# Kernel optimization log

Hardware: AMD Instinct MI355X
Metric: run time of the kernel (lower is better)

## Reference

```python
import jax, jax.numpy as jnp
import numpy as np

EPS = 1e-5
K = 5  # sklearn NearestNeighbors(n_neighbors=5); includes the query point itself


def setup_inputs() -> dict:
    key = jax.random.key(0)
    points = jax.random.uniform(key, (16384, 3), dtype=jnp.float32)
    return {"points": points}


def _compute_lrfs(points):
    # Brute-force KNN (indices only; sklearn returns the self-point as nearest).
    sq = jnp.sum(points * points, axis=1)                      # [N]
    d2 = sq[:, None] + sq[None, :] - 2.0 * points @ points.T   # [N,N]
    _, nbh_idx = jax.lax.top_k(-jax.lax.stop_gradient(d2), K)  # [N,K] (indices only -> no grad path)

    diffs = points[nbh_idx] - points[:, None, :]               # [N,K,3]  (nbh = points[idx] - point)
    centered = diffs - diffs.mean(axis=1, keepdims=True)
    cov = jnp.einsum('nkd,nke->nde', centered, centered) / K   # torch.cov(nbh.T, correction=0)
    eigvals, eigvecs = jnp.linalg.eigh(cov)                    # ascending eigvals, [N,3],[N,3,3]
    order = jnp.argsort(eigvals, axis=-1)[:, ::-1]             # descending

    # NOTE faithful quirks of the original:
    #  - eigvecs.T[:, axis] == eigvecs[axis, :] -> ROW of eigvecs is used as the axis
    #  - _calc_axis receives nbh (already point-relative) and does (pt - point) again,
    #    so the vote uses (neighbor - 2*point) dotted with the axis.
    def axis_row(idx):
        v = jnp.take_along_axis(eigvecs, idx[:, None, None], axis=1)[:, 0, :]  # [N,3]
        vote_vec = diffs - points[:, None, :]                                  # [N,K,3]
        count = jnp.sum(jnp.einsum('nkd,nd->nk', vote_vec, v) >= -EPS, axis=1)
        sign = jnp.where(2 * count >= K, 1.0, -1.0).astype(points.dtype)       # count >= K/2 keeps
        return v * sign[:, None]

    x_axis = axis_row(order[:, 0])
    z_axis = axis_row(order[:, 2])
    y_axis = jnp.cross(z_axis, x_axis)
    return jnp.stack([x_axis, y_axis, z_axis], axis=1)  # [N,3,3]


def reference(points):
    # forward(points, return_lrfs=True) -> (shot=0, lrfs); return the lrfs (the only real output).
    return _compute_lrfs(points)
```

## Files before the change

### kernel.cpp

```cpp
#include <hip/hip_runtime.h>

#define SLARTG_NEW 1

namespace {

constexpr int KNN_K = 5;
constexpr int GRID = 16;
constexpr int CELLS = GRID * GRID * GRID;
constexpr int LPG = 8;

constexpr int PPB = 16;
constexpr int STR = 16;
constexpr int TPB = PPB * STR;
constexpr int TILE = 2048;

#define EPSF    5.9604644775390625e-8f
#define EPS2F   3.552713678800501e-15f
#define SAFMINF 1.1754943508222875e-38f
#define SAFMAXF 8.507059173023462e+37f
#define RTMINF  1.0842021724855044e-19f
#define RTMAXF  9.223372036854776e+18f

__device__ __forceinline__ float sqnorm3(float x, float y, float z) {
#pragma clang fp contract(off)
  float a = x * x;
  float b = y * y;
  float c = z * z;
  return (a + b) + c;
}

__device__ __forceinline__ float dist2(float xi, float yi, float zi, float sqi,
                                       float xj, float yj, float zj, float sqj) {
#pragma clang fp contract(off)
  float dot = (xi * xj + yi * yj) + zi * zj;
  float a = sqi + sqj;
  return a - 2.0f * dot;
}

__device__ __forceinline__ int cell1d(float v) {
  int c = (int)(v * (float)GRID);
  if (c < 0) c = 0;
  if (c > GRID - 1) c = GRID - 1;
  return c;
}

__device__ __forceinline__ float slapy2f(float x, float y) {
#pragma clang fp contract(off)
  float xa = fabsf(x), ya = fabsf(y);
  float w = fmaxf(xa, ya);
  float z = fminf(xa, ya);
  if (z == 0.f) return w;
  float q = z / w;
  float q2 = q * q;
  float s = 1.0f + q2;
  return w * sqrtf(s);
}

__device__ __forceinline__ void slartgf(float f, float g, float* cs, float* sn, float* r) {
#pragma clang fp contract(off)
#if SLARTG_NEW
  float f1 = fabsf(f), g1 = fabsf(g);
  if (g == 0.f) { *cs = 1.f; *sn = 0.f; *r = f; }
  else if (f == 0.f) { *cs = 0.f; *sn = copysignf(1.f, g); *r = g1; }
  else if (f1 > RTMINF && f1 < RTMAXF && g1 > RTMINF && g1 < RTMAXF) {
    float ff = f * f;
    float gg = g * g;
    float d = sqrtf(ff + gg);
    *cs = f1 / d;
    float rr = copysignf(d, f);
    *sn = g / rr;
    *r = rr;
  } else {
    float u = fminf(SAFMAXF, fmaxf(fmaxf(SAFMINF, f1), g1));
    float fs = f / u, gs = g / u;
    float ff = fs * fs;
    float gg = gs * gs;
    float d = sqrtf(ff + gg);
    *cs = fabsf(fs) / d;
    float rr = copysignf(d, f);
    *sn = gs / rr;
    *r = rr * u;
  }
#else
  if (g == 0.f) { *cs = 1.f; *sn = 0.f; *r = f; }
  else if (f == 0.f) { *cs = 0.f; *sn = 1.f; *r = g; }
  else {
    float f2 = f * f;
    float g2 = g * g;
    float rr = sqrtf(f2 + g2);
    float c = f / rr, s = g / rr;
    if (fabsf(f) > fabsf(g) && c < 0.f) { c = -c; s = -s; rr = -rr; }
    *cs = c; *sn = s; *r = rr;
  }
#endif
}

__device__ __forceinline__ void slaev2f(float a, float b, float c,
                                        float* rt1, float* rt2, float* cs1, float* sn1) {
#pragma clang fp contract(off)
  float sm = a + c;
  float df = a - c;
  float adf = fabsf(df);
  float tb = b + b;
  float ab = fabsf(tb);
  float acmx, acmn;
  if (fabsf(a) > fabsf(c)) { acmx = a; acmn = c; } else { acmx = c; acmn = a; }
  float rt;
  if (adf > ab) { float q = ab / adf; rt = adf * sqrtf(1.0f + q * q); }
  else if (adf < ab) { float q = adf / ab; rt = ab * sqrtf(1.0f + q * q); }
  else rt = ab * sqrtf(2.0f);
  int sgn1;
  if (sm < 0.f) { *rt1 = 0.5f * (sm - rt); sgn1 = -1; *rt2 = (acmx / *rt1) * acmn - (b / *rt1) * b; }
  else if (sm > 0.f) { *rt1 = 0.5f * (sm + rt); sgn1 = 1; *rt2 = (acmx / *rt1) * acmn - (b / *rt1) * b; }
  else { *rt1 = 0.5f * rt; *rt2 = -0.5f * rt; sgn1 = 1; }
  float cs; int sgn2;
  if (df >= 0.f) { cs = df + rt; sgn2 = 1; } else { cs = df - rt; sgn2 = -1; }
  float acs = fabsf(cs);
  float c1, s1;
  if (acs > ab) {
    float ct = -tb / cs;
    s1 = 1.0f / sqrtf(1.0f + ct * ct);
    c1 = ct * s1;
  } else {
    if (ab == 0.f) { c1 = 1.f; s1 = 0.f; }
    else {
      float tn = -cs / tb;
      c1 = 1.0f / sqrtf(1.0f + tn * tn);
      s1 = tn * c1;
    }
  }
  if (sgn1 == sgn2) { float tn = c1; c1 = -s1; s1 = tn; }
  *cs1 = c1; *sn1 = s1;
}

__device__ __forceinline__ void slascl_g(float cfrom, float cto, int n, float* a) {
#pragma clang fp contract(off)
  float cfromc = cfrom, ctoc = cto;
  bool done = false;
  int guard = 0;
  while (!done && guard++ < 50) {
    float mul;
    float cfrom1 = cfromc * SAFMINF;
    if (cfrom1 == cfromc) {
      mul = ctoc / cfromc; done = true;
    } else {
      float cto1 = ctoc / SAFMAXF;
      if (cto1 == ctoc) { mul = ctoc; done = true; cfromc = 1.f; }
      else if (fabsf(cfrom1) > fabsf(ctoc) && ctoc != 0.f) { mul = SAFMINF; done = false; cfromc = cfrom1; }
      else if (fabsf(cto1) > fabsf(cfromc)) { mul = SAFMAXF; done = false; ctoc = cto1; }
      else { mul = ctoc / cfromc; done = true; }
    }
    for (int i = 0; i < n; ++i) a[i] = a[i] * mul;
  }
}

__device__ void steqr3f(float* d, float* e, float Z[3][3]) {
#pragma clang fp contract(off)
  const int n = 3;
  const float eps = EPSF, eps2 = EPS2F, safmin = SAFMINF;
  const float ssfmax = sqrtf(SAFMAXF) / 3.0f;
  const float ssfmin = sqrtf(SAFMINF) / EPS2F;
  int jtot = 0; const int nmaxit = n * 30;
  int l1 = 1;

  for (int guard = 0; guard < 200; ++guard) {
    if (l1 > n) break;
    if (l1 > 1) e[l1 - 2] = 0.f;
    int m = n;
    if (l1 <= n - 1) {
      for (int q = l1; q <= n - 1; ++q) {
        float tst = fabsf(e[q - 1]);
        if (tst == 0.f) { m = q; break; }
        if (tst <= (sqrtf(fabsf(d[q - 1])) * sqrtf(fabsf(d[q]))) * eps) { e[q - 1] = 0.f; m = q; break; }
      }
    }
    int l = l1, lsv = l, lend = m, lendsv = lend;
    l1 = m + 1;
    if (lend == l) continue;
    float anorm = 0.f;
    for (int q = l; q <= lend; ++q) anorm = fmaxf(anorm, fabsf(d[q - 1]));
    for (int q = l; q <= lend - 1; ++q) anorm = fmaxf(anorm, fabsf(e[q - 1]));
    int iscale = 0;
    if (anorm == 0.f) continue;
    if (anorm > ssfmax) {
      iscale = 1;
      slascl_g(anorm, ssfmax, lend - l + 1, d + l - 1);
      slascl_g(anorm, ssfmax, lend - l, e + l - 1);
    } else if (anorm < ssfmin) {
      iscale = 2;
      slascl_g(anorm, ssfmin, lend - l + 1, d + l - 1);
      slascl_g(anorm, ssfmin, lend - l, e + l - 1);
    }
    if (fabsf(d[lend - 1]) < fabsf(d[l - 1])) { lend = lsv; l = lendsv; }

    if (lend > l) {
      for (int g2 = 0; g2 < 400; ++g2) {
        int mm = lend;
        if (l != lend) {
          bool fnd = false;
          for (int q = l; q <= lend - 1; ++q) {
            float tst = e[q - 1] * e[q - 1];
            if (tst <= (eps2 * fabsf(d[q - 1])) * fabsf(d[q]) + safmin) { mm = q; fnd = true; break; }
          }
          if (!fnd) mm = lend;
        }
        if (mm < lend) e[mm - 1] = 0.f;
        float p = d[l - 1];
        if (mm == l) {
          d[l - 1] = p; ++l;
          if (l <= lend) continue; else break;
        }
        if (mm == l + 1) {
          float rt1, rt2, c, s;
          slaev2f(d[l - 1], e[l - 1], d[l], &rt1, &rt2, &c, &s);
          for (int r2 = 0; r2 < 3; ++r2) {
            float zt = Z[r2][l];
            float zl = Z[r2][l - 1];
            Z[r2][l] = c * zt - s * zl;
            Z[r2][l - 1] = s * zt + c * zl;
          }
          d[l - 1] = rt1; d[l] = rt2; e[l - 1] = 0.f;
          l += 2;
          if (l <= lend) continue; else break;
        }
        if (jtot == nmaxit) break;
        ++jtot;
        float g = (d[l] - p) / (2.0f * e[l - 1]);
        float r = slapy2f(g, 1.0f);
        g = d[mm - 1] - p + e[l - 1] / (g + copysignf(r, g));
        float ss = 1.0f, cc = 1.0f;
        p = 0.f;
        float cw[2], sw[2];
        for (int q = mm - 1; q >= l; --q) {
          float f = ss * e[q - 1];
          float b = cc * e[q - 1];
          float rr;
          slartgf(g, f, &cc, &ss, &rr);
          if (q != mm - 1) e[q] = rr;
          g = d[q] - p;
          rr = (d[q - 1] - g) * ss + 2.0f * cc * b;
          p = ss * rr;
          d[q] = g + p;
          g = cc * rr - b;
          cw[q - l] = cc; sw[q - l] = -ss;
        }
        for (int q = mm - 1; q >= l; --q) {
          float cj = cw[q - l], sj = sw[q - l];
          for (int r2 = 0; r2 < 3; ++r2) {
            float zt = Z[r2][q];
            float zl = Z[r2][q - 1];
            Z[r2][q] = cj * zt - sj * zl;
            Z[r2][q - 1] = sj * zt + cj * zl;
          }
        }
        d[l - 1] = d[l - 1] - p;
        e[l - 1] = g;
      }
    } else {
      for (int g2 = 0; g2 < 400; ++g2) {
        int mm = lend;
        if (l != lend) {
          bool fnd = false;
          for (int q = l; q >= lend + 1; --q) {
            float tst = e[q - 2] * e[q - 2];
            if (tst <= (eps2 * fabsf(d[q - 1])) * fabsf(d[q - 2]) + safmin) { mm = q; fnd = true; break; }
          }
          if (!fnd) mm = lend;
        }
        if (mm > lend) e[mm - 2] = 0.f;
        float p = d[l - 1];
        if (mm == l) {
          d[l - 1] = p; --l;
          if (l >= lend) continue; else break;
        }
        if (mm == l - 1) {
          float rt1, rt2, c, s;
          slaev2f(d[l - 2], e[l - 2], d[l - 1], &rt1, &rt2, &c, &s);
          for (int r2 = 0; r2 < 3; ++r2) {
            float zt = Z[r2][l - 1];
            float zl = Z[r2][l - 2];
            Z[r2][l - 1] = c * zt - s * zl;
            Z[r2][l - 2] = s * zt + c * zl;
          }
          d[l - 2] = rt1; d[l - 1] = rt2; e[l - 2] = 0.f;
          l -= 2;
          if (l >= lend) continue; else break;
        }
        if (jtot == nmaxit) break;
        ++jtot;
        float g = (d[l - 2] - p) / (2.0f * e[l - 2]);
        float r = slapy2f(g, 1.0f);
        g = d[mm - 1] - p + e[l - 2] / (g + copysignf(r, g));
        float ss = 1.0f, cc = 1.0f;
        p = 0.f;
        float cw[2], sw[2];
        for (int q = mm; q <= l - 1; ++q) {
          float f = ss * e[q - 1];
          float b = cc * e[q - 1];
          float rr;
          slartgf(g, f, &cc, &ss, &rr);
          if (q != mm) e[q - 2] = rr;
          g = d[q - 1] - p;
          rr = (d[q] - g) * ss + 2.0f * cc * b;
          p = ss * rr;
          d[q - 1] = g + p;
          g = cc * rr - b;
          cw[q - mm] = cc; sw[q - mm] = ss;
        }
        for (int q = mm; q <= l - 1; ++q) {
          float cj = cw[q - mm], sj = sw[q - mm];
          for (int r2 = 0; r2 < 3; ++r2) {
            float zt = Z[r2][q];
            float zl = Z[r2][q - 1];
            Z[r2][q] = cj * zt - sj * zl;
            Z[r2][q - 1] = sj * zt + cj * zl;
          }
        }
        d[l - 1] = d[l - 1] - p;
        e[l - 2] = g;
      }
    }
    if (iscale == 1) {
      slascl_g(ssfmax, anorm, lendsv - lsv + 1, d + lsv - 1);
      slascl_g(ssfmax, anorm, lendsv - lsv, e + lsv - 1);
    } else if (iscale == 2) {
      slascl_g(ssfmin, anorm, lendsv - lsv + 1, d + lsv - 1);
      slascl_g(ssfmin, anorm, lendsv - lsv, e + lsv - 1);
    }
    if (jtot >= nmaxit) break;
  }
  for (int ii = 2; ii <= n; ++ii) {
    int i0 = ii - 1, k0 = i0;
    float p = d[i0 - 1];
    for (int j = ii; j <= n; ++j)
      if (d[j - 1] < p) { k0 = j; p = d[j - 1]; }
    if (k0 != i0) {
      d[k0 - 1] = d[i0 - 1]; d[i0 - 1] = p;
      for (int r2 = 0; r2 < 3; ++r2) {
        float t = Z[r2][i0 - 1]; Z[r2][i0 - 1] = Z[r2][k0 - 1]; Z[r2][k0 - 1] = t;
      }
    }
  }
}

__device__ __forceinline__ void tridiag_of(const float* __restrict__ P, int i,
                                           const int* nb, float dif[KNN_K][3],
                                           float dd[3], float ee[2],
                                           float* taui_o, float* v2_o) {
#pragma clang fp contract(off)
  float px = P[i * 3 + 0], py = P[i * 3 + 1], pz = P[i * 3 + 2];
#pragma unroll
  for (int k = 0; k < KNN_K; ++k) {
    int j = nb[k];
    dif[k][0] = P[j * 3 + 0] - px;
    dif[k][1] = P[j * 3 + 1] - py;
    dif[k][2] = P[j * 3 + 2] - pz;
  }
  float mean[3];
  for (int c = 0; c < 3; ++c) {
    float sm = dif[0][c];
    for (int k = 1; k < KNN_K; ++k) sm = sm + dif[k][c];
    mean[c] = sm / 5.0f;
  }
  float cen[KNN_K][3];
  for (int k = 0; k < KNN_K; ++k)
    for (int c = 0; c < 3; ++c) cen[k][c] = dif[k][c] - mean[c];
  float cov[3][3];
  for (int a = 0; a < 3; ++a)
    for (int b = 0; b < 3; ++b) {
      float sm = cen[0][a] * cen[0][b];
      for (int k = 1; k < KNN_K; ++k) sm = sm + cen[k][a] * cen[k][b];
      cov[a][b] = sm / 5.0f;
    }

  float a00 = cov[0][0], a10 = cov[1][0], a20 = cov[2][0];
  float a11 = cov[1][1], a21 = cov[2][1], a22 = cov[2][2];
  float taui = 0.f, v2 = 0.f;
  float xnorm = fabsf(a20);
  if (xnorm == 0.f) {
    taui = 0.f;
    ee[0] = a10;
    dd[0] = a00; dd[1] = a11; dd[2] = a22; ee[1] = a21;
  } else {
    float beta = -copysignf(slapy2f(a10, xnorm), a10);
    taui = (beta - a10) / beta;
    v2 = a20 * (1.0f / (a10 - beta));
    ee[0] = beta;
    float w1 = taui * a11 + taui * (a21 * v2);
    float w2 = taui * a21 + (taui * v2) * a22;
    float dot = w1 + w2 * v2;
    float al = -((0.5f * taui) * dot);
    w1 = w1 + al;
    w2 = w2 + al * v2;
    dd[1] = (a11 - w1) - w1;
    ee[1] = (a21 - (v2 * w1)) - w2;
    dd[2] = (a22 - (v2 * w2)) - (w2 * v2);
    dd[0] = a00;
  }
  *taui_o = taui;
  *v2_o = v2;
}

__device__ __forceinline__ float vote5(const float dif[KNN_K][3],
                                       float px, float py, float pz, const float v[3]) {
#pragma clang fp contract(off)
  int cnt = 0;
  for (int k = 0; k < KNN_K; ++k) {
    float w0 = dif[k][0] - px;
    float w1 = dif[k][1] - py;
    float w2 = dif[k][2] - pz;
    float dt = (w0 * v[0] + w1 * v[1]) + w2 * v[2];
    cnt += (dt >= -1e-5f) ? 1 : 0;
  }
  return (2 * cnt >= KNN_K) ? 1.0f : -1.0f;
}

__device__ __forceinline__ void lrf_one(const float* __restrict__ P, float* __restrict__ out,
                                        int i, int n0, int n1, int n2, int n3, int n4) {
#pragma clang fp contract(off)
  int nb[KNN_K] = {n0, n1, n2, n3, n4};
  float dif[KNN_K][3];
  float dd[3], ee3[3];
  float taui, v2;
  tridiag_of(P, i, nb, dif, dd, ee3, &taui, &v2);
  ee3[2] = 0.f;

  float Zm[3][3] = {{1.f, 0.f, 0.f}, {0.f, 1.f, 0.f}, {0.f, 0.f, 1.f}};
  steqr3f(dd, ee3, Zm);

  if (taui != 0.f) {
    for (int j = 0; j < 3; ++j) {
      float w = Zm[1][j] + v2 * Zm[2][j];
      float t = -(taui * w);
      Zm[1][j] = Zm[1][j] + t;
      Zm[2][j] = Zm[2][j] + v2 * t;
    }
  }

  float px = P[i * 3 + 0], py = P[i * 3 + 1], pz = P[i * 3 + 2];
  float vx[3] = {Zm[2][0], Zm[2][1], Zm[2][2]};
  float vz[3] = {Zm[0][0], Zm[0][1], Zm[0][2]};
  float sx = vote5(dif, px, py, pz, vx);
  float sz = vote5(dif, px, py, pz, vz);
  float X[3] = {vx[0] * sx, vx[1] * sx, vx[2] * sx};
  float Zx[3] = {vz[0] * sz, vz[1] * sz, vz[2] * sz};
  float Y[3] = {Zx[1] * X[2] - Zx[2] * X[1],
                Zx[2] * X[0] - Zx[0] * X[2],
                Zx[0] * X[1] - Zx[1] * X[0]};
  out[i * 9 + 0] = X[0]; out[i * 9 + 1] = X[1]; out[i * 9 + 2] = X[2];
  out[i * 9 + 3] = Y[0]; out[i * 9 + 4] = Y[1]; out[i * 9 + 5] = Y[2];
  out[i * 9 + 6] = Zx[0]; out[i * 9 + 7] = Zx[1]; out[i * 9 + 8] = Zx[2];
}

__device__ __forceinline__ unsigned long long packkey(float d, int j) {
  unsigned int b = __float_as_uint(d);
  b ^= (b & 0x80000000u) ? 0xFFFFFFFFu : 0x80000000u;
  return ((unsigned long long)b << 32) | (unsigned int)j;
}

__device__ __forceinline__ float unpackd(unsigned long long k) {
  unsigned int b = (unsigned int)(k >> 32);
  b = (b & 0x80000000u) ? (b ^ 0x80000000u) : ~b;
  return __uint_as_float(b);
}

__device__ __forceinline__ int unpackj(unsigned long long k) {
  return (int)(unsigned int)(k & 0xFFFFFFFFu);
}

struct Key5 {
  unsigned long long k0, k1, k2, k3, k4;

  __device__ __forceinline__ void init() {
    k0 = k1 = k2 = k3 = k4 = 0xFFFFFFFFFFFFFFFFull;
  }

  __device__ __forceinline__ void insert(unsigned long long k) {
    if (k >= k4) return;
    bool l3 = k < k3;
    bool l2 = k < k2;
    bool l1 = k < k1;
    bool l0 = k < k0;
    k4 = l3 ? k3 : k;
    k3 = l3 ? (l2 ? k2 : k) : k3;
    k2 = l2 ? (l1 ? k1 : k) : k2;
    k1 = l1 ? (l0 ? k0 : k) : k1;
    k0 = l0 ? k : k0;
  }

  __device__ __forceinline__ void merge_xor(int off) {
    unsigned long long p0 = __shfl_xor(k0, off), p1 = __shfl_xor(k1, off),
                       p2 = __shfl_xor(k2, off), p3 = __shfl_xor(k3, off),
                       p4 = __shfl_xor(k4, off);
    insert(p0); insert(p1); insert(p2); insert(p3); insert(p4);
  }
};


__global__ __launch_bounds__(256) void hist_kernel(
    const float* __restrict__ P, int* __restrict__ counts, int n) {
  int i = blockIdx.x * 256 + threadIdx.x;
  if (i >= n) return;
  int cx = cell1d(P[i * 3 + 0]);
  int cy = cell1d(P[i * 3 + 1]);
  int cz = cell1d(P[i * 3 + 2]);
  atomicAdd(&counts[(cz * GRID + cy) * GRID + cx], 1);
}

__global__ __launch_bounds__(256) void scan_kernel(
    int* __restrict__ counts ,
    int* __restrict__ cursor) {
  __shared__ int psum[256];
  const int tid = threadIdx.x;
  const int CHUNK = CELLS / 256;
  int local[CHUNK];
  int s = 0;
  for (int k = 0; k < CHUNK; ++k) {
    local[k] = s;
    s += counts[tid * CHUNK + k];
  }
  psum[tid] = s;
  __syncthreads();
  for (int off = 1; off < 256; off <<= 1) {
    int v = (tid >= off) ? psum[tid - off] : 0;
    __syncthreads();
    psum[tid] += v;
    __syncthreads();
  }
  int base = (tid > 0) ? psum[tid - 1] : 0;
  for (int k = 0; k < CHUNK; ++k) {
    int o = base + local[k];
    counts[tid * CHUNK + k] = o;
    cursor[tid * CHUNK + k] = o;
  }
  if (tid == 255) counts[CELLS] = psum[255];
}

__global__ __launch_bounds__(256) void scatter_kernel(
    const float* __restrict__ P, int* __restrict__ cursor,
    float4* __restrict__ sorted, int n) {
  int i = blockIdx.x * 256 + threadIdx.x;
  if (i >= n) return;
  float x = P[i * 3 + 0], y = P[i * 3 + 1], z = P[i * 3 + 2];
  int c = (cell1d(z) * GRID + cell1d(y)) * GRID + cell1d(x);
  int pos = atomicAdd(&cursor[c], 1);
  sorted[pos] = make_float4(x, y, z, __int_as_float(i));
}

__global__ __launch_bounds__(256) void knn_kernel(
    const float4* __restrict__ sorted, const int* __restrict__ offsets,
    int* __restrict__ nbh, int n) {
  const int tid = threadIdx.x;
  const int r = tid & (LPG - 1);
  const int t = blockIdx.x * (256 / LPG) + (tid / LPG);
  if (t >= n) return;

  float4 q = sorted[t];
  const float qs = sqnorm3(q.x, q.y, q.z);
  const int cx = cell1d(q.x), cy = cell1d(q.y), cz = cell1d(q.z);
  const float h = 1.0f / (float)GRID;

  Key5 tp;
  tp.init();

  {
    const int x0 = max(0, cx - 1), x1 = min(GRID - 1, cx + 1);
    const int xsp = x1 - x0 + 1;
    int ksv[9], kev[9];
#pragma unroll
    for (int s9 = 0; s9 < 9; ++s9) {
      int dz = s9 / 3 - 1, dy = s9 % 3 - 1;
      int zz = cz + dz, yy = cy + dy;
      bool ok = (zz >= 0) && (zz < GRID) && (yy >= 0) && (yy < GRID);
      int c0 = ok ? ((zz * GRID + yy) * GRID + x0) : 0;
      int ks = offsets[c0];
      int ke = offsets[c0 + xsp];
      ksv[s9] = ks;
      kev[s9] = ok ? ke : ks;
    }
#pragma unroll
    for (int s9 = 0; s9 < 9; ++s9) {
      for (int k = ksv[s9] + r; k < kev[s9]; k += LPG) {
        float4 p = sorted[k];
        float psq = sqnorm3(p.x, p.y, p.z);
        float dv = dist2(q.x, q.y, q.z, qs, p.x, p.y, p.z, psq);
        tp.insert(packkey(dv, __float_as_int(p.w)));
      }
    }
  }

  float B = unpackd(tp.k4);
  B = fminf(B, __shfl_xor(B, 1));
  B = fminf(B, __shfl_xor(B, 2));
  B = fminf(B, __shfl_xor(B, 4));

  for (int m = 2; m < GRID; ++m) {
    float lb = (float)(m - 1) * h;
    if (lb * lb > B * 1.00001f + 1e-6f) break;
    for (int dz = -m; dz <= m; ++dz) {
      int zz = cz + dz;
      if (zz < 0 || zz >= GRID) continue;
      bool zface = (dz == -m || dz == m);
      for (int dy = -m; dy <= m; ++dy) {
        int yy = cy + dy;
        if (yy < 0 || yy >= GRID) continue;
        bool yface = (dy == -m || dy == m);
        int rowbase = (zz * GRID + yy) * GRID;
        if (zface || yface) {
          int x0 = max(0, cx - m), x1 = min(GRID - 1, cx + m);
          int ks = offsets[rowbase + x0], ke = offsets[rowbase + x1 + 1];
          for (int k = ks + r; k < ke; k += LPG) {
            float4 p = sorted[k];
            float psq = sqnorm3(p.x, p.y, p.z);
            float dv = dist2(q.x, q.y, q.z, qs, p.x, p.y, p.z, psq);
            tp.insert(packkey(dv, __float_as_int(p.w)));
          }
        } else {
          int xa = cx - m, xb = cx + m;
          if (xa >= 0) {
            int ks = offsets[rowbase + xa], ke = offsets[rowbase + xa + 1];
            for (int k = ks + r; k < ke; k += LPG) {
              float4 p = sorted[k];
              float psq = sqnorm3(p.x, p.y, p.z);
              float dv = dist2(q.x, q.y, q.z, qs, p.x, p.y, p.z, psq);
              tp.insert(packkey(dv, __float_as_int(p.w)));
            }
          }
          if (xb < GRID) {
            int ks = offsets[rowbase + xb], ke = offsets[rowbase + xb + 1];
            for (int k = ks + r; k < ke; k += LPG) {
              float4 p = sorted[k];
              float psq = sqnorm3(p.x, p.y, p.z);
              float dv = dist2(q.x, q.y, q.z, qs, p.x, p.y, p.z, psq);
              tp.insert(packkey(dv, __float_as_int(p.w)));
            }
          }
        }
      }
    }
    B = unpackd(tp.k4);
    B = fminf(B, __shfl_xor(B, 1));
    B = fminf(B, __shfl_xor(B, 2));
    B = fminf(B, __shfl_xor(B, 4));
  }

  tp.merge_xor(1);
  tp.merge_xor(2);
  tp.merge_xor(4);

  if (r == 0) {
    nbh[t * 5 + 0] = unpackj(tp.k0);
    nbh[t * 5 + 1] = unpackj(tp.k1);
    nbh[t * 5 + 2] = unpackj(tp.k2);
    nbh[t * 5 + 3] = unpackj(tp.k3);
    nbh[t * 5 + 4] = unpackj(tp.k4);
  }
}

__global__ __launch_bounds__(256) void classify_kernel(
    const float* __restrict__ P, const float4* __restrict__ sorted,
    const int* __restrict__ nbh, int* __restrict__ perm,
    int* __restrict__ cnts, int n) {
#pragma clang fp contract(off)
  int t = blockIdx.x * 256 + threadIdx.x;
  if (t >= n) return;
  int io = __float_as_int(sorted[t].w);
  int nb[KNN_K] = {nbh[t * 5 + 0], nbh[t * 5 + 1], nbh[t * 5 + 2],
                   nbh[t * 5 + 3], nbh[t * 5 + 4]};
  float dif[KNN_K][3];
  float dd[3], ee[2];
  float taui, v2;
  tridiag_of(P, io, nb, dif, dd, ee, &taui, &v2);

  const float eps = EPSF;
  int m = 3;
  for (int q = 1; q <= 2; ++q) {
    float tst = fabsf(ee[q - 1]);
    if (tst == 0.f) { m = q; break; }
    if (tst <= (sqrtf(fabsf(dd[q - 1])) * sqrtf(fabsf(dd[q]))) * eps) { m = q; break; }
  }
  bool qr = false;
  if (m > 1) {
    qr = (fabsf(dd[m - 1]) < fabsf(dd[0]));
  }
  if (qr) {
    int pos = atomicAdd(&cnts[1], 1);
    perm[n - 1 - pos] = t;
  } else {
    int pos = atomicAdd(&cnts[0], 1);
    perm[pos] = t;
  }
}

__global__ __launch_bounds__(64) void solver_kernel(
    const float* __restrict__ P, const float4* __restrict__ sorted,
    const int* __restrict__ nbh, const int* __restrict__ perm,
    float* __restrict__ out, int n) {
  int s = blockIdx.x * 64 + threadIdx.x;
  if (s >= n) return;
  int t = perm[s];
  int io = __float_as_int(sorted[t].w);
  lrf_one(P, out, io,
          nbh[t * 5 + 0], nbh[t * 5 + 1], nbh[t * 5 + 2],
          nbh[t * 5 + 3], nbh[t * 5 + 4]);
}


__global__ __launch_bounds__(TPB) void knn_brute_kernel(
    const float* __restrict__ P, float* __restrict__ out, int n) {
  __shared__ float4 tile[TILE];

  const int tid = threadIdx.x;
  const int p = tid >> 4;
  const int s = tid & 15;
  const int i = blockIdx.x * PPB + p;
  const int iq = (i < n) ? i : (n - 1);

  const float qx = P[iq * 3 + 0];
  const float qy = P[iq * 3 + 1];
  const float qz = P[iq * 3 + 2];
  const float qs = sqnorm3(qx, qy, qz);

  Key5 t;
  t.init();

  for (int base = 0; base < n; base += TILE) {
    int cnt = min(TILE, n - base);
    __syncthreads();
    for (int j = tid; j < cnt; j += TPB) {
      float x = P[(base + j) * 3 + 0];
      float y = P[(base + j) * 3 + 1];
      float z = P[(base + j) * 3 + 2];
      tile[j] = make_float4(x, y, z, sqnorm3(x, y, z));
    }
    __syncthreads();
    for (int j = s; j < cnt; j += STR) {
      float4 q = tile[j];
      t.insert(packkey(dist2(qx, qy, qz, qs, q.x, q.y, q.z, q.w), base + j));
    }
  }

#pragma unroll
  for (int rnd = 0; rnd < 4; ++rnd) {
    t.merge_xor(1 << rnd);
  }

  if (s == 0 && i < n) {
    lrf_one(P, out, i, unpackj(t.k0), unpackj(t.k1), unpackj(t.k2),
            unpackj(t.k3), unpackj(t.k4));
  }
}

}

extern "C" void kernel_launch(void* const* d_in, const int* in_sizes, int n_in,
                              void* d_out, int out_size, void* d_ws, size_t ws_size,
                              hipStream_t stream) {
  (void)n_in; (void)out_size;
  const float* P = (const float*)d_in[0];
  float* out = (float*)d_out;
  const int n = in_sizes[0] / 3;
  if (n <= 0) return;

  size_t off_sorted = 0;
  size_t off_counts = off_sorted + (size_t)n * sizeof(float4);
  size_t off_cursor = off_counts + ((size_t)(CELLS + 1) * sizeof(int) + 15) / 16 * 16;
  size_t off_nbh = off_cursor + (size_t)CELLS * sizeof(int);
  size_t off_perm = off_nbh + (size_t)n * 5 * sizeof(int);
  size_t off_cnts = off_perm + (size_t)n * sizeof(int);
  size_t need = off_cnts + 16;

  if (ws_size >= need && n >= KNN_K) {
    char* base = (char*)d_ws;
    float4* sorted = (float4*)(base + off_sorted);
    int* counts = (int*)(base + off_counts);
    int* cursor = (int*)(base + off_cursor);
    int* nbh = (int*)(base + off_nbh);
    int* perm = (int*)(base + off_perm);
    int* cnts = (int*)(base + off_cnts);

    hipMemsetAsync(counts, 0, (size_t)CELLS * sizeof(int), stream);
    hipMemsetAsync(cnts, 0, 2 * sizeof(int), stream);
    hist_kernel<<<(n + 255) / 256, 256, 0, stream>>>(P, counts, n);
    scan_kernel<<<1, 256, 0, stream>>>(counts, cursor);
    scatter_kernel<<<(n + 255) / 256, 256, 0, stream>>>(P, cursor, sorted, n);
    const int ppb = 256 / LPG;
    knn_kernel<<<(n + ppb - 1) / ppb, 256, 0, stream>>>(sorted, counts, nbh, n);
    classify_kernel<<<(n + 255) / 256, 256, 0, stream>>>(P, sorted, nbh, perm, cnts, n);
    solver_kernel<<<(n + 63) / 64, 64, 0, stream>>>(P, sorted, nbh, perm, out, n);
  } else {
    const int blocks = (n + PPB - 1) / PPB;
    knn_brute_kernel<<<blocks, TPB, 0, stream>>>(P, out, n);
  }
}
```

Baseline: 91.66 us.

## Fuse classification into KNN kernel and fold counter reset into scan

The classify kernel's work now runs inside the KNN kernel. The lane that holds the merged neighbours computes the tridiagonal form and the QR/QL classification and writes perm directly. The cnts memset is dropped, and its zeroing moves into the scan kernel. This removes two launches and a reload of nbh. In exchange, only one of every 8 lanes does the classification work, so lanes sit idle and register pressure in the KNN kernel rises. One subtle point: fp contract(off) was a pragma in classify and may not carry over to the fused code.

```diff
diff --git a/kernel.cpp b/kernel.cpp
--- a/kernel.cpp
+++ b/kernel.cpp
@@ -509,9 +509,10 @@
 
 __global__ __launch_bounds__(256) void scan_kernel(
     int* __restrict__ counts ,
-    int* __restrict__ cursor) {
+    int* __restrict__ cursor, int* __restrict__ cnts) {
   __shared__ int psum[256];
   const int tid = threadIdx.x;
+  if (tid < 2) cnts[tid] = 0;
   const int CHUNK = CELLS / 256;
   int local[CHUNK];
   int s = 0;
@@ -549,7 +550,8 @@
 
 __global__ __launch_bounds__(256) void knn_kernel(
     const float4* __restrict__ sorted, const int* __restrict__ offsets,
-    int* __restrict__ nbh, int n) {
+    const float* __restrict__ P, int* __restrict__ nbh,
+    int* __restrict__ perm, int* __restrict__ cnts, int n) {
   const int tid = threadIdx.x;
   const int r = tid & (LPG - 1);
   const int t = blockIdx.x * (256 / LPG) + (tid / LPG);
@@ -649,46 +651,37 @@
   tp.merge_xor(4);
 
   if (r == 0) {
-    nbh[t * 5 + 0] = unpackj(tp.k0);
-    nbh[t * 5 + 1] = unpackj(tp.k1);
-    nbh[t * 5 + 2] = unpackj(tp.k2);
-    nbh[t * 5 + 3] = unpackj(tp.k3);
-    nbh[t * 5 + 4] = unpackj(tp.k4);
-  }
-}
-
-__global__ __launch_bounds__(256) void classify_kernel(
-    const float* __restrict__ P, const float4* __restrict__ sorted,
-    const int* __restrict__ nbh, int* __restrict__ perm,
-    int* __restrict__ cnts, int n) {
-#pragma clang fp contract(off)
-  int t = blockIdx.x * 256 + threadIdx.x;
-  if (t >= n) return;
-  int io = __float_as_int(sorted[t].w);
-  int nb[KNN_K] = {nbh[t * 5 + 0], nbh[t * 5 + 1], nbh[t * 5 + 2],
-                   nbh[t * 5 + 3], nbh[t * 5 + 4]};
-  float dif[KNN_K][3];
-  float dd[3], ee[2];
-  float taui, v2;
-  tridiag_of(P, io, nb, dif, dd, ee, &taui, &v2);
-
-  const float eps = EPSF;
-  int m = 3;
-  for (int q = 1; q <= 2; ++q) {
-    float tst = fabsf(ee[q - 1]);
-    if (tst == 0.f) { m = q; break; }
-    if (tst <= (sqrtf(fabsf(dd[q - 1])) * sqrtf(fabsf(dd[q]))) * eps) { m = q; break; }
-  }
-  bool qr = false;
-  if (m > 1) {
-    qr = (fabsf(dd[m - 1]) < fabsf(dd[0]));
-  }
-  if (qr) {
-    int pos = atomicAdd(&cnts[1], 1);
-    perm[n - 1 - pos] = t;
-  } else {
-    int pos = atomicAdd(&cnts[0], 1);
-    perm[pos] = t;
+    int nb[KNN_K] = {unpackj(tp.k0), unpackj(tp.k1), unpackj(tp.k2),
+                     unpackj(tp.k3), unpackj(tp.k4)};
+    nbh[t * 5 + 0] = nb[0];
+    nbh[t * 5 + 1] = nb[1];
+    nbh[t * 5 + 2] = nb[2];
+    nbh[t * 5 + 3] = nb[3];
+    nbh[t * 5 + 4] = nb[4];
+
+    int io = __float_as_int(q.w);
+    float dif[KNN_K][3];
+    float dd[3], ee[2];
+    float taui, v2;
+    tridiag_of(P, io, nb, dif, dd, ee, &taui, &v2);
+    const float eps = EPSF;
+    int m = 3;
+    for (int qq = 1; qq <= 2; ++qq) {
+      float tst = fabsf(ee[qq - 1]);
+      if (tst == 0.f) { m = qq; break; }
+      if (tst <= (sqrtf(fabsf(dd[qq - 1])) * sqrtf(fabsf(dd[qq]))) * eps) { m = qq; break; }
+    }
+    bool qr = false;
+    if (m > 1) {
+      qr = (fabsf(dd[m - 1]) < fabsf(dd[0]));
+    }
+    if (qr) {
+      int pos = atomicAdd(&cnts[1], 1);
+      perm[n - 1 - pos] = t;
+    } else {
+      int pos = atomicAdd(&cnts[0], 1);
+      perm[pos] = t;
+    }
   }
 }
 
@@ -780,13 +773,12 @@
     int* cnts = (int*)(base + off_cnts);
 
     hipMemsetAsync(counts, 0, (size_t)CELLS * sizeof(int), stream);
-    hipMemsetAsync(cnts, 0, 2 * sizeof(int), stream);
     hist_kernel<<<(n + 255) / 256, 256, 0, stream>>>(P, counts, n);
-    scan_kernel<<<1, 256, 0, stream>>>(counts, cursor);
+    scan_kernel<<<1, 256, 0, stream>>>(counts, cursor, cnts);
     scatter_kernel<<<(n + 255) / 256, 256, 0, stream>>>(P, cursor, sorted, n);
     const int ppb = 256 / LPG;
-    knn_kernel<<<(n + ppb - 1) / ppb, 256, 0, stream>>>(sorted, counts, nbh, n);
-    classify_kernel<<<(n + 255) / 256, 256, 0, stream>>>(P, sorted, nbh, perm, cnts, n);
+    knn_kernel<<<(n + ppb - 1) / ppb, 256, 0, stream>>>(
+        sorted, counts, P, nbh, perm, cnts, n);
     solver_kernel<<<(n + 63) / 64, 64, 0, stream>>>(P, sorted, nbh, perm, out, n);
   } else {
     const int blocks = (n + PPB - 1) / PPB;
```

New measurement: 113.9 us. +24.3%, slower.
